# Kernel optimization log

Measured on AMD Instinct MI355X. Metric: run time of the kernel, lower is better.

Reference implementation:

```python
import jax, jax.numpy as jnp
import numpy as np

N, E, F, HID, HEADS, NC = 50000, 800000, 128, 32, 8, 10
SLOPE = 0.2  # PyG GATConv default negative_slope


def setup_inputs() -> dict:
    key = jax.random.key(0)
    ks = jax.random.split(key, 12)
    return {
        "x": jax.random.normal(ks[0], (N, F), jnp.float32),
        "edge_index": jax.random.randint(ks[1], (2, E), 0, N, jnp.int64),
        "W1": jax.random.normal(ks[2], (F, HEADS * HID), jnp.float32) * 0.05,
        "as1": jax.random.normal(ks[3], (HEADS, HID), jnp.float32) * 0.05,
        "ad1": jax.random.normal(ks[4], (HEADS, HID), jnp.float32) * 0.05,
        "b1": jnp.zeros((HEADS * HID,), jnp.float32),
        "W2": jax.random.normal(ks[5], (HEADS * HID, HID), jnp.float32) * 0.05,
        "as2": jax.random.normal(ks[6], (1, HID), jnp.float32) * 0.05,
        "ad2": jax.random.normal(ks[7], (1, HID), jnp.float32) * 0.05,
        "b2": jnp.zeros((HID,), jnp.float32),
        "Wl": jax.random.normal(ks[8], (HID, NC), jnp.float32) * 0.05,
        "bl": jnp.zeros((NC,), jnp.float32),
    }


def _gat_conv(x, src, dst, W, a_src, a_dst, b):
    # x: [N, Fin], W: [Fin, H*C], a_src/a_dst: [H, C]
    H, C = a_src.shape
    h = (x @ W).reshape(-1, H, C)                    # [N, H, C]
    alpha_s = jnp.einsum('nhc,hc->nh', h, a_src)      # [N, H]
    alpha_d = jnp.einsum('nhc,hc->nh', h, a_dst)      # [N, H]
    e = jax.nn.leaky_relu(alpha_s[src] + alpha_d[dst], SLOPE)  # [Etot, H]
    # segment softmax over incoming edges of each dst node
    m = jax.ops.segment_max(e, dst, num_segments=N)   # [N, H]
    ex = jnp.exp(e - m[dst])
    s = jax.ops.segment_sum(ex, dst, num_segments=N)  # [N, H]
    w = ex / (s[dst] + 1e-16)                         # [Etot, H]
    out = jax.ops.segment_sum(h[src] * w[:, :, None], dst, num_segments=N)  # [N, H, C]
    return out.reshape(-1, H * C) + b


def reference(x, edge_index, W1, as1, ad1, b1, W2, as2, ad2, b2, Wl, bl):
    # add self loops (PyG GATConv default add_self_loops=True)
    loops = jnp.arange(N, dtype=edge_index.dtype)
    src = jnp.concatenate([edge_index[0], loops])
    dst = jnp.concatenate([edge_index[1], loops])
    h = _gat_conv(x, src, dst, W1, as1, ad1, b1)   # [N, 8*32], concat heads
    h = jax.nn.elu(h)
    # dropout p=0.1 is a no-op in eval mode
    h = _gat_conv(h, src, dst, W2, as2, ad2, b2)   # [N, 32], single head
    h = jax.nn.elu(h)
    return h @ Wl + bl                              # [N, 10]
```

## Files before the change

kernel.cpp:

```cpp
#include <hip/hip_runtime.h>
#include <hip/hip_bf16.h>
#include <math.h>

#define N_NODES 50000
#define NEDGES  800000
#define ETOT    (NEDGES + N_NODES)
#define FIN     128
#define HID     32
#define HEADS   8
#define F1      (HEADS * HID)
#define NC      10
#define SLOPE   0.2f

__device__ __forceinline__ float leaky(float x) { return x > 0.f ? x : SLOPE * x; }
__device__ __forceinline__ float elu_f(float x) { return x > 0.f ? x : expm1f(x); }

__device__ __forceinline__ unsigned short f2bf(float f) {
    unsigned int u = __float_as_uint(f);
    u = (u + 0x7fffu + ((u >> 16) & 1u)) >> 16;
    return (unsigned short)u;
}
__device__ __forceinline__ float bflo(unsigned int u) {
    return __uint_as_float(u << 16);
}
__device__ __forceinline__ float bfhi(unsigned int u) {
    return __uint_as_float(u & 0xffff0000u);
}

__global__ void k_detect(const void* ei, int* flag) {
    const long long* p = (const long long*)ei;
    long long bad = 0;
#pragma unroll
    for (int i = 0; i < 8; ++i) {
        long long v = p[i];
        bad |= (v < 0 || v >= N_NODES) ? 1 : 0;
    }
    *flag = (bad == 0);
}

__device__ __forceinline__ int load_edge(const void* eiv, int is64, int idx) {
    if (is64) return (int)((const long long*)eiv)[idx];
    return ((const int*)eiv)[idx];
}

__global__ void k_deg(const void* eiv, const int* __restrict__ flag,
                      int* __restrict__ deg) {
    int i = blockIdx.x * blockDim.x + threadIdx.x;
    if (i >= ETOT) return;
    int d = (i < NEDGES) ? load_edge(eiv, *flag, NEDGES + i) : (i - NEDGES);
    atomicAdd(&deg[d], 1);
}

__global__ __launch_bounds__(1024) void k_scan(const int* __restrict__ deg,
                                               int* __restrict__ rowptr) {
    __shared__ int ssum[1024];
    __shared__ int s_carry;
    int tid = threadIdx.x;
    if (tid == 0) s_carry = 0;
    __syncthreads();
    const int PER  = 8;
    const int TILE = 1024 * PER;
    for (int base = 0; base < N_NODES; base += TILE) {
        int i0 = base + tid * PER;
        int v[PER];
        int tsum = 0;
#pragma unroll
        for (int k = 0; k < PER; ++k) {
            int i = i0 + k;
            v[k] = (i < N_NODES) ? deg[i] : 0;
            tsum += v[k];
        }
        ssum[tid] = tsum;
        __syncthreads();
        for (int off = 1; off < 1024; off <<= 1) {
            int t = (tid >= off) ? ssum[tid - off] : 0;
            __syncthreads();
            ssum[tid] += t;
            __syncthreads();
        }
        int excl = s_carry + ssum[tid] - tsum;
#pragma unroll
        for (int k = 0; k < PER; ++k) {
            int i = i0 + k;
            if (i < N_NODES) rowptr[i] = excl;
            excl += v[k];
        }
        __syncthreads();
        if (tid == 0) s_carry += ssum[1023];
        __syncthreads();
    }
    if (tid == 0) rowptr[N_NODES] = s_carry;
}

__global__ void k_fill(const void* eiv, const int* __restrict__ flag,
                       const int* __restrict__ rowptr, int* __restrict__ fill,
                       int* __restrict__ col) {
    int i = blockIdx.x * blockDim.x + threadIdx.x;
    if (i >= ETOT) return;
    int s, d;
    if (i < NEDGES) {
        int is64 = *flag;
        s = load_edge(eiv, is64, i);
        d = load_edge(eiv, is64, NEDGES + i);
    } else {
        s = i - NEDGES;
        d = s;
    }
    int pos = rowptr[d] + atomicAdd(&fill[d], 1);
    col[pos] = s;
}

__global__ __launch_bounds__(256) void k_gemm1(
    const float4* __restrict__ x4, const float* __restrict__ W1,
    const float* __restrict__ as1, const float* __restrict__ ad1,
    unsigned short* __restrict__ h1b, float* __restrict__ alpha_s,
    float* __restrict__ alpha_d) {
    __shared__ float xs[32][FIN];
    int tid = threadIdx.x;
    int node0 = blockIdx.x * 32;
    for (int idx = tid; idx < 32 * 32; idx += 256) {
        int m = idx >> 5, k4 = idx & 31;
        int n = node0 + m;
        float4 v = (n < N_NODES) ? x4[(size_t)n * 32 + k4] : float4{0.f, 0.f, 0.f, 0.f};
        *(float4*)&xs[m][k4 * 4] = v;
    }
    __syncthreads();
    int c0 = tid & 127;
    int mbase = (tid >> 7) * 16;
    float accA[16], accB[16];
#pragma unroll
    for (int m = 0; m < 16; ++m) { accA[m] = 0.f; accB[m] = 0.f; }
    for (int k = 0; k < FIN; k += 4) {
        float wa0 = W1[(k + 0) * F1 + c0];
        float wa1 = W1[(k + 1) * F1 + c0];
        float wa2 = W1[(k + 2) * F1 + c0];
        float wa3 = W1[(k + 3) * F1 + c0];
        float wb0 = W1[(k + 0) * F1 + c0 + 128];
        float wb1 = W1[(k + 1) * F1 + c0 + 128];
        float wb2 = W1[(k + 2) * F1 + c0 + 128];
        float wb3 = W1[(k + 3) * F1 + c0 + 128];
#pragma unroll
        for (int m = 0; m < 16; ++m) {
            float4 xv = *(const float4*)&xs[mbase + m][k];
            accA[m] = fmaf(xv.x, wa0, accA[m]);
            accA[m] = fmaf(xv.y, wa1, accA[m]);
            accA[m] = fmaf(xv.z, wa2, accA[m]);
            accA[m] = fmaf(xv.w, wa3, accA[m]);
            accB[m] = fmaf(xv.x, wb0, accB[m]);
            accB[m] = fmaf(xv.y, wb1, accB[m]);
            accB[m] = fmaf(xv.z, wb2, accB[m]);
            accB[m] = fmaf(xv.w, wb3, accB[m]);
        }
    }
    int headA = c0 >> 5, headB = headA + 4;
    int cc = c0 & 31;
    float aAs = as1[headA * HID + cc], aAd = ad1[headA * HID + cc];
    float aBs = as1[headB * HID + cc], aBd = ad1[headB * HID + cc];
#pragma unroll
    for (int m = 0; m < 16; ++m) {
        int n = node0 + mbase + m;
        if (n >= N_NODES) break;
        h1b[(size_t)n * F1 + c0]       = f2bf(accA[m]);
        h1b[(size_t)n * F1 + c0 + 128] = f2bf(accB[m]);
        float vsA = accA[m] * aAs, vdA = accA[m] * aAd;
        float vsB = accB[m] * aBs, vdB = accB[m] * aBd;
#pragma unroll
        for (int off = 16; off >= 1; off >>= 1) {
            vsA += __shfl_xor(vsA, off, 64);
            vdA += __shfl_xor(vdA, off, 64);
            vsB += __shfl_xor(vsB, off, 64);
            vdB += __shfl_xor(vdB, off, 64);
        }
        if (cc == 0) {
            alpha_s[n * HEADS + headA] = vsA;
            alpha_d[n * HEADS + headA] = vdA;
            alpha_s[n * HEADS + headB] = vsB;
            alpha_d[n * HEADS + headB] = vdB;
        }
    }
}

__global__ __launch_bounds__(256) void k_agg1(
    const uint2* __restrict__ h1u, const float* __restrict__ a_s,
    const float* __restrict__ a_d, const int* __restrict__ rowptr,
    const int* __restrict__ col, const float4* __restrict__ b1,
    float4* __restrict__ hout) {
    int tid = threadIdx.x;
    int lane = tid & 63;
    int n = blockIdx.x * 4 + (tid >> 6);
    if (n >= N_NODES) return;
    int head = lane >> 3;
    int start = rowptr[n], end = rowptr[n + 1];
    float adv = a_d[n * HEADS + head];
    float4 acc = {0.f, 0.f, 0.f, 0.f};
    float ssum = 0.f;
    int j = start;
    for (; j + 3 < end; j += 4) {
        int s0 = col[j], s1 = col[j + 1], s2 = col[j + 2], s3 = col[j + 3];
        uint2 g0 = h1u[(size_t)s0 * 64 + lane];
        uint2 g1 = h1u[(size_t)s1 * 64 + lane];
        uint2 g2 = h1u[(size_t)s2 * 64 + lane];
        uint2 g3 = h1u[(size_t)s3 * 64 + lane];
        float w0 = expf(leaky(a_s[s0 * HEADS + head] + adv));
        float w1 = expf(leaky(a_s[s1 * HEADS + head] + adv));
        float w2 = expf(leaky(a_s[s2 * HEADS + head] + adv));
        float w3 = expf(leaky(a_s[s3 * HEADS + head] + adv));
        acc.x = fmaf(w0, bflo(g0.x), acc.x); acc.y = fmaf(w0, bfhi(g0.x), acc.y);
        acc.z = fmaf(w0, bflo(g0.y), acc.z); acc.w = fmaf(w0, bfhi(g0.y), acc.w);
        acc.x = fmaf(w1, bflo(g1.x), acc.x); acc.y = fmaf(w1, bfhi(g1.x), acc.y);
        acc.z = fmaf(w1, bflo(g1.y), acc.z); acc.w = fmaf(w1, bfhi(g1.y), acc.w);
        acc.x = fmaf(w2, bflo(g2.x), acc.x); acc.y = fmaf(w2, bfhi(g2.x), acc.y);
        acc.z = fmaf(w2, bflo(g2.y), acc.z); acc.w = fmaf(w2, bfhi(g2.y), acc.w);
        acc.x = fmaf(w3, bflo(g3.x), acc.x); acc.y = fmaf(w3, bfhi(g3.x), acc.y);
        acc.z = fmaf(w3, bflo(g3.y), acc.z); acc.w = fmaf(w3, bfhi(g3.y), acc.w);
        ssum += (w0 + w1) + (w2 + w3);
    }
    for (; j < end; ++j) {
        int s0 = col[j];
        uint2 g0 = h1u[(size_t)s0 * 64 + lane];
        float w0 = expf(leaky(a_s[s0 * HEADS + head] + adv));
        acc.x = fmaf(w0, bflo(g0.x), acc.x); acc.y = fmaf(w0, bfhi(g0.x), acc.y);
        acc.z = fmaf(w0, bflo(g0.y), acc.z); acc.w = fmaf(w0, bfhi(g0.y), acc.w);
        ssum += w0;
    }
    float inv = 1.f / ssum;
    float4 b = b1[lane];
    float4 o;
    o.x = elu_f(fmaf(acc.x, inv, b.x));
    o.y = elu_f(fmaf(acc.y, inv, b.y));
    o.z = elu_f(fmaf(acc.z, inv, b.z));
    o.w = elu_f(fmaf(acc.w, inv, b.w));
    hout[(size_t)n * 64 + lane] = o;
}

__global__ __launch_bounds__(256) void k_gemm2(
    const float4* __restrict__ hin4, const float* __restrict__ W2,
    const float* __restrict__ as2, const float* __restrict__ ad2,
    float* __restrict__ h2, float* __restrict__ alpha_s, float* __restrict__ alpha_d) {
    __shared__ float hs[16][F1 + 4];
    int tid = threadIdx.x;
    int node0 = blockIdx.x * 16;
    for (int idx = tid; idx < 16 * 64; idx += 256) {
        int m = idx >> 6, k4 = idx & 63;
        int n = node0 + m;
        float4 v = (n < N_NODES) ? hin4[(size_t)n * 64 + k4] : float4{0.f, 0.f, 0.f, 0.f};
        *(float4*)&hs[m][k4 * 4] = v;
    }
    __syncthreads();
    int c = tid & 15;
    int m = tid >> 4;
    float acc0 = 0.f, acc1 = 0.f;
    for (int k = 0; k < F1; k += 4) {
        float w00 = W2[(k + 0) * HID + c];
        float w01 = W2[(k + 1) * HID + c];
        float w02 = W2[(k + 2) * HID + c];
        float w03 = W2[(k + 3) * HID + c];
        float w10 = W2[(k + 0) * HID + c + 16];
        float w11 = W2[(k + 1) * HID + c + 16];
        float w12 = W2[(k + 2) * HID + c + 16];
        float w13 = W2[(k + 3) * HID + c + 16];
        float4 xv = *(const float4*)&hs[m][k];
        acc0 = fmaf(xv.w, w03, fmaf(xv.z, w02, fmaf(xv.y, w01, fmaf(xv.x, w00, acc0))));
        acc1 = fmaf(xv.w, w13, fmaf(xv.z, w12, fmaf(xv.y, w11, fmaf(xv.x, w10, acc1))));
    }
    int n = node0 + m;
    if (n < N_NODES) {
        h2[(size_t)n * HID + c]      = acc0;
        h2[(size_t)n * HID + c + 16] = acc1;
        float vs = acc0 * as2[c] + acc1 * as2[c + 16];
        float vd = acc0 * ad2[c] + acc1 * ad2[c + 16];
#pragma unroll
        for (int off = 8; off >= 1; off >>= 1) {
            vs += __shfl_xor(vs, off, 64);
            vd += __shfl_xor(vd, off, 64);
        }
        if (c == 0) {
            alpha_s[n] = vs;
            alpha_d[n] = vd;
        }
    }
}

__global__ __launch_bounds__(256) void k_agg2(
    const float* __restrict__ h2, const float* __restrict__ a_s,
    const float* __restrict__ a_d, const int* __restrict__ rowptr,
    const int* __restrict__ col, const float* __restrict__ b2,
    float* __restrict__ hout) {
    int tid = threadIdx.x;
    int ml = tid >> 5, c = tid & 31;
    int n = blockIdx.x * 8 + ml;
    if (n >= N_NODES) return;
    int start = rowptr[n], end = rowptr[n + 1];
    float adv = a_d[n];
    float ssum = 0.f, acc = 0.f;
    int j = start;
    for (; j + 1 < end; j += 2) {
        int s0 = col[j], s1 = col[j + 1];
        float v0 = h2[(size_t)s0 * HID + c];
        float v1 = h2[(size_t)s1 * HID + c];
        float w0 = expf(leaky(a_s[s0] + adv));
        float w1 = expf(leaky(a_s[s1] + adv));
        acc = fmaf(w0, v0, acc);
        acc = fmaf(w1, v1, acc);
        ssum += w0 + w1;
    }
    if (j < end) {
        int s0 = col[j];
        float w0 = expf(leaky(a_s[s0] + adv));
        acc = fmaf(w0, h2[(size_t)s0 * HID + c], acc);
        ssum += w0;
    }
    hout[(size_t)n * HID + c] = elu_f(acc / ssum + b2[c]);
}

__global__ void k_final(const float* __restrict__ hf, const float* __restrict__ Wl,
                        const float* __restrict__ bl, float* __restrict__ out) {
    int n = blockIdx.x * blockDim.x + threadIdx.x;
    if (n >= N_NODES) return;
    float h[HID];
    const float4* hp = (const float4*)(hf + (size_t)n * HID);
#pragma unroll
    for (int i = 0; i < 8; ++i) {
        float4 v = hp[i];
        h[4 * i] = v.x; h[4 * i + 1] = v.y; h[4 * i + 2] = v.z; h[4 * i + 3] = v.w;
    }
#pragma unroll
    for (int j = 0; j < NC; ++j) {
        float acc = bl[j];
#pragma unroll
        for (int c = 0; c < HID; ++c) acc += h[c] * Wl[c * NC + j];
        out[(size_t)n * NC + j] = acc;
    }
}

extern "C" void kernel_launch(void* const* d_in, const int* in_sizes, int n_in,
                              void* d_out, int out_size, void* d_ws, size_t ws_size,
                              hipStream_t stream) {
    (void)in_sizes; (void)n_in; (void)out_size; (void)ws_size;
    const float* x   = (const float*)d_in[0];
    const void*  ei  = d_in[1];
    const float* W1  = (const float*)d_in[2];
    const float* as1 = (const float*)d_in[3];
    const float* ad1 = (const float*)d_in[4];
    const float* b1  = (const float*)d_in[5];
    const float* W2  = (const float*)d_in[6];
    const float* as2 = (const float*)d_in[7];
    const float* ad2 = (const float*)d_in[8];
    const float* b2  = (const float*)d_in[9];
    const float* Wl  = (const float*)d_in[10];
    const float* bl  = (const float*)d_in[11];
    float* out = (float*)d_out;

    char* ws = (char*)d_ws;
    size_t off = 0;
    auto alloc = [&](size_t bytes) {
        void* p = ws + off;
        off += (bytes + 255) & ~size_t(255);
        return p;
    };
    int*   flag    = (int*)alloc(4);
    int*   deg     = (int*)alloc(N_NODES * 4);
    int*   fill    = (int*)alloc(N_NODES * 4);
    int*   rowptr  = (int*)alloc((N_NODES + 1) * 4);
    int*   col     = (int*)alloc(ETOT * 4);
    unsigned short* h1b = (unsigned short*)alloc((size_t)N_NODES * F1 * 2);
    float* as1n    = (float*)alloc(N_NODES * HEADS * 4);
    float* ad1n    = (float*)alloc(N_NODES * HEADS * 4);
    float* hin2    = (float*)alloc((size_t)N_NODES * F1 * 4);
    float* h2      = (float*)alloc((size_t)N_NODES * HID * 4);
    float* as2n    = (float*)alloc(N_NODES * 4);
    float* ad2n    = (float*)alloc(N_NODES * 4);
    float* h2f     = (float*)h1b;

    hipMemsetAsync(deg, 0, N_NODES * 4, stream);
    hipMemsetAsync(fill, 0, N_NODES * 4, stream);

    k_detect<<<1, 1, 0, stream>>>(ei, flag);

    int egrid = (ETOT + 255) / 256;
    k_deg<<<egrid, 256, 0, stream>>>(ei, flag, deg);
    k_scan<<<1, 1024, 0, stream>>>(deg, rowptr);
    k_fill<<<egrid, 256, 0, stream>>>(ei, flag, rowptr, fill, col);

    k_gemm1<<<(N_NODES + 31) / 32, 256, 0, stream>>>((const float4*)x, W1, as1, ad1,
                                                     h1b, as1n, ad1n);
    k_agg1<<<(N_NODES + 3) / 4, 256, 0, stream>>>((const uint2*)h1b, as1n, ad1n, rowptr,
                                                  col, (const float4*)b1, (float4*)hin2);
    k_gemm2<<<(N_NODES + 15) / 16, 256, 0, stream>>>((const float4*)hin2, W2, as2, ad2,
                                                     h2, as2n, ad2n);
    k_agg2<<<(N_NODES + 7) / 8, 256, 0, stream>>>(h2, as2n, ad2n, rowptr, col, b2, h2f);
    k_final<<<(N_NODES + 255) / 256, 256, 0, stream>>>(h2f, Wl, bl, out);
}
```

Measured before the change: 435.5 us.

## Parallelize CSR scan, prefetch W1 in gemm1, fuse final linear into agg2

Replaces the single-block serial prefix scan over node degrees with a three-kernel multi-block scan built on wave shuffles. Software-pipelines the W1 loads in the first GEMM by fetching the next k-slice before the FMAs on the current one. Fuses the final linear layer into the second aggregation kernel through shared memory, removing one launch and the intermediate hidden-state round trip. The fused kernel drops its bounds check and relies on N being divisible by 8, and the scan hardcodes 49 blocks for N.

```diff
diff --git a/kernel.cpp b/kernel.cpp
--- a/kernel.cpp
+++ b/kernel.cpp
@@ -11,6 +11,7 @@
 #define F1      (HEADS * HID)
 #define NC      10
 #define SLOPE   0.2f
+#define SCB     49
 
 __device__ __forceinline__ float leaky(float x) { return x > 0.f ? x : SLOPE * x; }
 __device__ __forceinline__ float elu_f(float x) { return x > 0.f ? x : expm1f(x); }
@@ -20,12 +21,8 @@
     u = (u + 0x7fffu + ((u >> 16) & 1u)) >> 16;
     return (unsigned short)u;
 }
-__device__ __forceinline__ float bflo(unsigned int u) {
-    return __uint_as_float(u << 16);
-}
-__device__ __forceinline__ float bfhi(unsigned int u) {
-    return __uint_as_float(u & 0xffff0000u);
-}
+__device__ __forceinline__ float bflo(unsigned int u) { return __uint_as_float(u << 16); }
+__device__ __forceinline__ float bfhi(unsigned int u) { return __uint_as_float(u & 0xffff0000u); }
 
 __global__ void k_detect(const void* ei, int* flag) {
     const long long* p = (const long long*)ei;
@@ -51,45 +48,71 @@
     atomicAdd(&deg[d], 1);
 }
 
-__global__ __launch_bounds__(1024) void k_scan(const int* __restrict__ deg,
-                                               int* __restrict__ rowptr) {
-    __shared__ int ssum[1024];
-    __shared__ int s_carry;
-    int tid = threadIdx.x;
-    if (tid == 0) s_carry = 0;
+__global__ __launch_bounds__(256) void k_scan_a(const int* __restrict__ deg,
+                                                int* __restrict__ bsum) {
+    int b = blockIdx.x, t = threadIdx.x;
+    int base = b * 1024 + t * 4;
+    int s = 0;
+#pragma unroll
+    for (int i = 0; i < 4; ++i) {
+        int idx = base + i;
+        s += (idx < N_NODES) ? deg[idx] : 0;
+    }
+#pragma unroll
+    for (int off = 32; off >= 1; off >>= 1) s += __shfl_xor(s, off, 64);
+    __shared__ int ws[4];
+    int lane = t & 63, w = t >> 6;
+    if (lane == 0) ws[w] = s;
     __syncthreads();
-    const int PER  = 8;
-    const int TILE = 1024 * PER;
-    for (int base = 0; base < N_NODES; base += TILE) {
-        int i0 = base + tid * PER;
-        int v[PER];
-        int tsum = 0;
-#pragma unroll
-        for (int k = 0; k < PER; ++k) {
-            int i = i0 + k;
-            v[k] = (i < N_NODES) ? deg[i] : 0;
-            tsum += v[k];
-        }
-        ssum[tid] = tsum;
-        __syncthreads();
-        for (int off = 1; off < 1024; off <<= 1) {
-            int t = (tid >= off) ? ssum[tid - off] : 0;
-            __syncthreads();
-            ssum[tid] += t;
-            __syncthreads();
-        }
-        int excl = s_carry + ssum[tid] - tsum;
-#pragma unroll
-        for (int k = 0; k < PER; ++k) {
-            int i = i0 + k;
-            if (i < N_NODES) rowptr[i] = excl;
-            excl += v[k];
-        }
-        __syncthreads();
-        if (tid == 0) s_carry += ssum[1023];
-        __syncthreads();
-    }
-    if (tid == 0) rowptr[N_NODES] = s_carry;
+    if (t == 0) bsum[b] = ws[0] + ws[1] + ws[2] + ws[3];
+}
+
+__global__ void k_scan_b(const int* __restrict__ bsum, int* __restrict__ boff,
+                         int* __restrict__ rowptr) {
+    int lane = threadIdx.x;
+    int v = (lane < SCB) ? bsum[lane] : 0;
+    int inc = v;
+#pragma unroll
+    for (int off = 1; off < 64; off <<= 1) {
+        int up = __shfl_up(inc, off, 64);
+        if (lane >= off) inc += up;
+    }
+    if (lane < SCB) boff[lane] = inc - v;
+    if (lane == 63) rowptr[N_NODES] = inc;
+}
+
+__global__ __launch_bounds__(256) void k_scan_c(const int* __restrict__ deg,
+                                                const int* __restrict__ boff,
+                                                int* __restrict__ rowptr) {
+    int b = blockIdx.x, t = threadIdx.x;
+    int base = b * 1024 + t * 4;
+    int v[4];
+    int ts = 0;
+#pragma unroll
+    for (int i = 0; i < 4; ++i) {
+        int idx = base + i;
+        v[i] = (idx < N_NODES) ? deg[idx] : 0;
+        ts += v[i];
+    }
+    int inc = ts;
+#pragma unroll
+    for (int off = 1; off < 64; off <<= 1) {
+        int up = __shfl_up(inc, off, 64);
+        if ((t & 63) >= off) inc += up;
+    }
+    __shared__ int ws[4];
+    int lane = t & 63, w = t >> 6;
+    if (lane == 63) ws[w] = inc;
+    __syncthreads();
+    int woff = 0;
+    for (int i = 0; i < w; ++i) woff += ws[i];
+    int excl = boff[b] + woff + inc - ts;
+#pragma unroll
+    for (int i = 0; i < 4; ++i) {
+        int idx = base + i;
+        if (idx < N_NODES) rowptr[idx] = excl;
+        excl += v[i];
+    }
 }
 
 __global__ void k_fill(const void* eiv, const int* __restrict__ flag,
@@ -130,28 +153,41 @@
     float accA[16], accB[16];
 #pragma unroll
     for (int m = 0; m < 16; ++m) { accA[m] = 0.f; accB[m] = 0.f; }
-    for (int k = 0; k < FIN; k += 4) {
-        float wa0 = W1[(k + 0) * F1 + c0];
-        float wa1 = W1[(k + 1) * F1 + c0];
-        float wa2 = W1[(k + 2) * F1 + c0];
-        float wa3 = W1[(k + 3) * F1 + c0];
-        float wb0 = W1[(k + 0) * F1 + c0 + 128];
-        float wb1 = W1[(k + 1) * F1 + c0 + 128];
-        float wb2 = W1[(k + 2) * F1 + c0 + 128];
-        float wb3 = W1[(k + 3) * F1 + c0 + 128];
-#pragma unroll
-        for (int m = 0; m < 16; ++m) {
-            float4 xv = *(const float4*)&xs[mbase + m][k];
-            accA[m] = fmaf(xv.x, wa0, accA[m]);
-            accA[m] = fmaf(xv.y, wa1, accA[m]);
-            accA[m] = fmaf(xv.z, wa2, accA[m]);
-            accA[m] = fmaf(xv.w, wa3, accA[m]);
-            accB[m] = fmaf(xv.x, wb0, accB[m]);
-            accB[m] = fmaf(xv.y, wb1, accB[m]);
-            accB[m] = fmaf(xv.z, wb2, accB[m]);
-            accB[m] = fmaf(xv.w, wb3, accB[m]);
-        }
-    }
+
+#define LOADW(A, B, KK)                                   \
+    {                                                     \
+        const float* _p = W1 + (KK) * F1 + c0;            \
+        A[0] = _p[0 * F1]; A[1] = _p[1 * F1];             \
+        A[2] = _p[2 * F1]; A[3] = _p[3 * F1];             \
+        B[0] = _p[0 * F1 + 128]; B[1] = _p[1 * F1 + 128]; \
+        B[2] = _p[2 * F1 + 128]; B[3] = _p[3 * F1 + 128]; \
+    }
+#define FMAS(KK, A, B)                                                \
+    _Pragma("unroll") for (int m = 0; m < 16; ++m) {                  \
+        float4 xv = *(const float4*)&xs[mbase + m][KK];               \
+        accA[m] = fmaf(xv.x, A[0], accA[m]);                          \
+        accA[m] = fmaf(xv.y, A[1], accA[m]);                          \
+        accA[m] = fmaf(xv.z, A[2], accA[m]);                          \
+        accA[m] = fmaf(xv.w, A[3], accA[m]);                          \
+        accB[m] = fmaf(xv.x, B[0], accB[m]);                          \
+        accB[m] = fmaf(xv.y, B[1], accB[m]);                          \
+        accB[m] = fmaf(xv.z, B[2], accB[m]);                          \
+        accB[m] = fmaf(xv.w, B[3], accB[m]);                          \
+    }
+
+    float ca[4], cb[4];
+    LOADW(ca, cb, 0);
+    for (int k = 0; k < FIN - 4; k += 4) {
+        float na[4], nb[4];
+        LOADW(na, nb, k + 4);
+        FMAS(k, ca, cb);
+#pragma unroll
+        for (int j = 0; j < 4; ++j) { ca[j] = na[j]; cb[j] = nb[j]; }
+    }
+    FMAS(FIN - 4, ca, cb);
+#undef LOADW
+#undef FMAS
+
     int headA = c0 >> 5, headB = headA + 4;
     int cc = c0 & 31;
     float aAs = as1[headA * HID + cc], aAd = ad1[headA * HID + cc];
@@ -285,11 +321,12 @@
     const float* __restrict__ h2, const float* __restrict__ a_s,
     const float* __restrict__ a_d, const int* __restrict__ rowptr,
     const int* __restrict__ col, const float* __restrict__ b2,
-    float* __restrict__ hout) {
+    const float* __restrict__ Wl, const float* __restrict__ bl,
+    float* __restrict__ out) {
+    __shared__ float sh[8][HID];
     int tid = threadIdx.x;
     int ml = tid >> 5, c = tid & 31;
     int n = blockIdx.x * 8 + ml;
-    if (n >= N_NODES) return;
     int start = rowptr[n], end = rowptr[n + 1];
     float adv = a_d[n];
     float ssum = 0.f, acc = 0.f;
@@ -310,26 +347,15 @@
         acc = fmaf(w0, h2[(size_t)s0 * HID + c], acc);
         ssum += w0;
     }
-    hout[(size_t)n * HID + c] = elu_f(acc / ssum + b2[c]);
-}
-
-__global__ void k_final(const float* __restrict__ hf, const float* __restrict__ Wl,
-                        const float* __restrict__ bl, float* __restrict__ out) {
-    int n = blockIdx.x * blockDim.x + threadIdx.x;
-    if (n >= N_NODES) return;
-    float h[HID];
-    const float4* hp = (const float4*)(hf + (size_t)n * HID);
-#pragma unroll
-    for (int i = 0; i < 8; ++i) {
-        float4 v = hp[i];
-        h[4 * i] = v.x; h[4 * i + 1] = v.y; h[4 * i + 2] = v.z; h[4 * i + 3] = v.w;
-    }
-#pragma unroll
-    for (int j = 0; j < NC; ++j) {
-        float acc = bl[j];
-#pragma unroll
-        for (int c = 0; c < HID; ++c) acc += h[c] * Wl[c * NC + j];
-        out[(size_t)n * NC + j] = acc;
+    sh[ml][c] = elu_f(acc / ssum + b2[c]);
+    __syncthreads();
+    if (tid < 8 * NC) {
+        int nl = tid / NC, jj = tid - nl * NC;
+        float o = bl[jj];
+#pragma unroll
+        for (int cc = 0; cc < HID; ++cc)
+            o = fmaf(sh[nl][cc], Wl[cc * NC + jj], o);
+        out[(size_t)(blockIdx.x * 8 + nl) * NC + jj] = o;
     }
 }
 
@@ -362,6 +388,8 @@
     int*   deg     = (int*)alloc(N_NODES * 4);
     int*   fill    = (int*)alloc(N_NODES * 4);
     int*   rowptr  = (int*)alloc((N_NODES + 1) * 4);
+    int*   bsum    = (int*)alloc(SCB * 4);
+    int*   boff    = (int*)alloc(SCB * 4);
     int*   col     = (int*)alloc(ETOT * 4);
     unsigned short* h1b = (unsigned short*)alloc((size_t)N_NODES * F1 * 2);
     float* as1n    = (float*)alloc(N_NODES * HEADS * 4);
@@ -370,7 +398,6 @@
     float* h2      = (float*)alloc((size_t)N_NODES * HID * 4);
     float* as2n    = (float*)alloc(N_NODES * 4);
     float* ad2n    = (float*)alloc(N_NODES * 4);
-    float* h2f     = (float*)h1b;
 
     hipMemsetAsync(deg, 0, N_NODES * 4, stream);
     hipMemsetAsync(fill, 0, N_NODES * 4, stream);
@@ -379,7 +406,9 @@
 
     int egrid = (ETOT + 255) / 256;
     k_deg<<<egrid, 256, 0, stream>>>(ei, flag, deg);
-    k_scan<<<1, 1024, 0, stream>>>(deg, rowptr);
+    k_scan_a<<<SCB, 256, 0, stream>>>(deg, bsum);
+    k_scan_b<<<1, 64, 0, stream>>>(bsum, boff, rowptr);
+    k_scan_c<<<SCB, 256, 0, stream>>>(deg, boff, rowptr);
     k_fill<<<egrid, 256, 0, stream>>>(ei, flag, rowptr, fill, col);
 
     k_gemm1<<<(N_NODES + 31) / 32, 256, 0, stream>>>((const float4*)x, W1, as1, ad1,
@@ -388,6 +417,6 @@
                                                   col, (const float4*)b1, (float4*)hin2);
     k_gemm2<<<(N_NODES + 15) / 16, 256, 0, stream>>>((const float4*)hin2, W2, as2, ad2,
                                                      h2, as2n, ad2n);
-    k_agg2<<<(N_NODES + 7) / 8, 256, 0, stream>>>(h2, as2n, ad2n, rowptr, col, b2, h2f);
-    k_final<<<(N_NODES + 255) / 256, 256, 0, stream>>>(h2f, Wl, bl, out);
-}
+    k_agg2<<<N_NODES / 8, 256, 0, stream>>>(h2, as2n, ad2n, rowptr, col, b2,
+                                            Wl, bl, out);
+}
```

After: 423.5 us. 2.7% less time.
